# Optimization experiments

Hardware: AMD Instinct MI355X
Metric: run time of the kernel (lower is better)

## Reference

```python
import jax, jax.numpy as jnp
import numpy as np

DIM = 1024
NUM_HEADS = 16
HEAD_DIM = DIM // NUM_HEADS
SCALE = HEAD_DIM ** -0.5


def setup_inputs() -> dict:
    key = jax.random.key(0)
    ks = jax.random.split(key, 7)
    s = DIM ** -0.5
    return {
        "x": jax.random.normal(ks[0], (4, 2048, DIM), dtype=jnp.float32),
        "wq": jax.random.normal(ks[1], (DIM, DIM), dtype=jnp.float32) * s,
        "wk": jax.random.normal(ks[2], (DIM, DIM), dtype=jnp.float32) * s,
        "wv": jax.random.normal(ks[3], (DIM, DIM), dtype=jnp.float32) * s,
        "wo": jax.random.normal(ks[4], (DIM, DIM), dtype=jnp.float32) * s,
        "bo": jax.random.normal(ks[5], (DIM,), dtype=jnp.float32) * 0.02,
    }


def reference(x, wq, wk, wv, wo, bo):
    B, N, C = x.shape
    H, D = NUM_HEADS, HEAD_DIM
    # projections (qkv_bias=False); weights stored as [out, in] like nn.Linear
    q = jnp.einsum("bnc,oc->bno", x, wq).reshape(B, N, H, D).transpose(0, 2, 1, 3)
    k = jnp.einsum("bnc,oc->bno", x, wk).reshape(B, N, H, D).transpose(0, 2, 1, 3)
    v = jnp.einsum("bnc,oc->bno", x, wv).reshape(B, N, H, D).transpose(0, 2, 1, 3)
    # full NxN scores, scaled after the matmul as in the original
    scores = jnp.einsum("bhqd,bhkd->bhqk", q, k) * SCALE
    probs = jax.nn.softmax(scores, axis=-1)  # attn_drop is identity (p=0, eval)
    out = jnp.einsum("bhqk,bhkd->bhqd", probs, v)
    out = out.transpose(0, 2, 1, 3).reshape(B, N, C)
    # output projection with bias; proj_drop identity
    return jnp.einsum("bnc,oc->bno", out, wo) + bo
```

## Files before the change

kernel.cpp:

```cpp
#include <hip/hip_runtime.h>

typedef unsigned short u16;
typedef __attribute__((ext_vector_type(8))) short short8;
typedef __attribute__((ext_vector_type(4))) float f32x4;
typedef __attribute__((ext_vector_type(2))) unsigned u32x2;
typedef __attribute__((ext_vector_type(4))) unsigned u32x4;

#define LOG2E 1.44269504088896340736f

__device__ __forceinline__ u16 f2bf(float f) {
    unsigned u = __float_as_uint(f);
    u += 0x7fffu + ((u >> 16) & 1u);
    return (u16)(u >> 16);
}

__device__ __forceinline__ void async_cp16(const void* g, void* l) {
    __builtin_amdgcn_global_load_lds(
        (const __attribute__((address_space(1))) unsigned*)g,
        (__attribute__((address_space(3))) unsigned*)l, 16, 0, 0);
}

__device__ __forceinline__ unsigned pack_trunc(float a, float b) {
    return __builtin_amdgcn_perm(__float_as_uint(b), __float_as_uint(a), 0x07060302u);
}

__global__ void cast_all(const float4* __restrict__ x,
                         const float4* __restrict__ wq, const float4* __restrict__ wk,
                         const float4* __restrict__ wv, const float4* __restrict__ wo,
                         uint2* __restrict__ xb, uint2* __restrict__ wqkv,
                         uint2* __restrict__ wob) {
    long long g = (long long)blockIdx.x * blockDim.x + threadIdx.x;
    const long long XG = (8192LL * 1024) / 4;
    const long long WN = (1024LL * 1024) / 4;
    float4 v;
    uint2* dst;
    if (g < XG) {
        v = x[g];
        dst = xb + g;
    } else {
        long long t = g - XG;
        int s = (int)(t / WN);
        long long r = t - (long long)s * WN;
        const float4* src = (s == 0) ? wq : (s == 1) ? wk : (s == 2) ? wv : wo;
        v = src[r];
        dst = (s < 3) ? (wqkv + (long long)s * WN + r) : (wob + r);
    }
    uint2 p;
    p.x = (unsigned)f2bf(v.x) | ((unsigned)f2bf(v.y) << 16);
    p.y = (unsigned)f2bf(v.z) | ((unsigned)f2bf(v.w) << 16);
    *dst = p;
}

template <int MODE>
__global__ __launch_bounds__(256, 2) void gemm_nt(
    const u16* __restrict__ A, const u16* __restrict__ Bw,
    u16* __restrict__ Qo, u16* __restrict__ Ko, u16* __restrict__ Vto,
    float* __restrict__ Fo, const float* __restrict__ bias, int K) {
    __shared__ u16 As[128 * 64];
    __shared__ u16 Bs[128 * 64];

    const int tid = threadIdx.x;
    const int lane = tid & 63, wave = tid >> 6;
    const int wm = wave >> 1, wn = wave & 1;
    const int quad = lane >> 4, l16 = lane & 15;
    const long long m0 = (long long)blockIdx.x * 128;
    const long long n0 = (long long)blockIdx.y * 128;

    f32x4 acc[4][4];
#pragma unroll
    for (int i = 0; i < 4; i++)
#pragma unroll
        for (int j = 0; j < 4; j++) acc[i][j] = (f32x4){0.f, 0.f, 0.f, 0.f};

    for (int kt = 0; kt < K; kt += 64) {
#pragma unroll
        for (int i = 0; i < 4; i++) {
            int ff = i * 256 + tid;
            int row = ff >> 3, c = ff & 7;
            int gc = c ^ (row & 7);
            async_cp16(A + (m0 + row) * K + kt + gc * 8, &As[ff * 8]);
            async_cp16(Bw + (n0 + row) * K + kt + gc * 8, &Bs[ff * 8]);
        }
        __syncthreads();
#pragma unroll
        for (int ks = 0; ks < 2; ks++) {
            short8 af[4], bfr[4];
#pragma unroll
            for (int t = 0; t < 4; t++) {
                int rowA = wm * 64 + t * 16 + l16;
                int ca = (ks * 4 + quad) ^ (rowA & 7);
                af[t] = *(const short8*)(&As[rowA * 64 + ca * 8]);
                int rowB = wn * 64 + t * 16 + l16;
                int cb = (ks * 4 + quad) ^ (rowB & 7);
                bfr[t] = *(const short8*)(&Bs[rowB * 64 + cb * 8]);
            }
#pragma unroll
            for (int i = 0; i < 4; i++)
#pragma unroll
                for (int j = 0; j < 4; j++)
                    acc[i][j] = __builtin_amdgcn_mfma_f32_16x16x32_bf16(
                        af[i], bfr[j], acc[i][j], 0, 0, 0);
        }
        __syncthreads();
    }

#pragma unroll
    for (int i = 0; i < 4; i++) {
        int mg = (int)m0 + wm * 64 + i * 16 + quad * 4;
#pragma unroll
        for (int j = 0; j < 4; j++) {
            int ng = (int)n0 + wn * 64 + j * 16 + l16;
            f32x4 v = acc[i][j];
            if (MODE == 0) {
                int which = ng >> 10;
                int wi = ng & 1023;
                int h = wi >> 6, d = wi & 63;
                int b = mg >> 11;
                int seq = mg & 2047;
                long long bh = (long long)(b * 16 + h);
                if (which == 0) {
                    const float QS = 0.125f * LOG2E;
                    u16* dst = Qo + (bh * 2048 + seq) * 64 + d;
#pragma unroll
                    for (int r = 0; r < 4; r++) dst[r * 64] = f2bf(v[r] * QS);
                } else if (which == 1) {
                    u16* dst = Ko + (bh * 2048 + seq) * 64 + d;
#pragma unroll
                    for (int r = 0; r < 4; r++) dst[r * 64] = f2bf(v[r]);
                } else {
                    u16* dst = Vto + (bh * 64 + d) * 2048 + seq;
                    uint2 p;
                    p.x = (unsigned)f2bf(v[0]) | ((unsigned)f2bf(v[1]) << 16);
                    p.y = (unsigned)f2bf(v[2]) | ((unsigned)f2bf(v[3]) << 16);
                    *(uint2*)dst = p;
                }
            } else {
                float* dst = Fo + (long long)mg * 1024 + ng;
                float bb = bias[ng];
#pragma unroll
                for (int r = 0; r < 4; r++) dst[r * 1024] = v[r] + bb;
            }
        }
    }
}

__global__ __launch_bounds__(512, 4) void attn(
    const u16* __restrict__ Q, const u16* __restrict__ Kb,
    const u16* __restrict__ Vt, u16* __restrict__ O) {
    __shared__ u16 Ks[2][128 * 64];
    __shared__ u16 Vs[2][128 * 64];

    const int tid = threadIdx.x;
    const int lane = tid & 63, wave = tid >> 6;
    const int quad = lane >> 4, l16 = lane & 15;
    const int qt = blockIdx.y, bh = blockIdx.x;

    const u16* Qh = Q + (long long)bh * 2048 * 64;
    const u16* Kh = Kb + (long long)bh * 2048 * 64;
    const u16* Vh = Vt + (long long)bh * 64 * 2048;
    const int q0 = qt * 256 + wave * 32;

    const int srow = tid >> 3, sc = tid & 7;
    const int sgc = sc ^ (srow & 7);
    const u16* Kg = Kh + srow * 64 + sgc * 8;
    const u16* Vg = Vh + (long long)srow * 2048 + sgc * 8;

    short8 qf[2][2];
#pragma unroll
    for (int tm = 0; tm < 2; tm++)
#pragma unroll
        for (int ks = 0; ks < 2; ks++)
            qf[tm][ks] = *(const short8*)(Qh + (q0 + tm * 16 + l16) * 64 + ks * 32 + quad * 8);

    int kvo[2][4];
#pragma unroll
    for (int ks = 0; ks < 2; ks++)
#pragma unroll
        for (int tn = 0; tn < 4; tn++) {
            int row = tn * 16 + l16;
            kvo[ks][tn] = row * 64 + (((ks * 4 + quad) ^ (row & 7)) * 8);
        }

    f32x4 o_acc[2][4], lacc[2];
#pragma unroll
    for (int tm = 0; tm < 2; tm++) {
        lacc[tm] = (f32x4){0.f, 0.f, 0.f, 0.f};
#pragma unroll
        for (int tn = 0; tn < 4; tn++) o_acc[tm][tn] = (f32x4){0.f, 0.f, 0.f, 0.f};
    }
    const float NEGC = -12.0f * LOG2E;
    const short BF1 = (short)0x3F80;
    const short8 ones = {BF1, BF1, BF1, BF1, BF1, BF1, BF1, BF1};

    async_cp16(Kg, &Ks[0][tid * 8]);
    async_cp16(Kg + 4096, &Ks[0][4096 + tid * 8]);
    async_cp16(Vg, &Vs[0][tid * 8]);
    async_cp16(Vg + 64, &Vs[0][4096 + tid * 8]);

#define ATTN_HALF(KC, VC)                                                               \
    do {                                                                                \
        const u16* Kc = (KC);                                                           \
        const u16* Vc = (VC);                                                           \
        f32x4 s[2][4];                                                                  \
        _Pragma("unroll") for (int tm = 0; tm < 2; tm++)                                \
            _Pragma("unroll") for (int tn = 0; tn < 4; tn++)                            \
                s[tm][tn] = (f32x4){NEGC, NEGC, NEGC, NEGC};                            \
        _Pragma("unroll") for (int ks = 0; ks < 2; ks++) {                              \
            short8 kf[4];                                                               \
            _Pragma("unroll") for (int tn = 0; tn < 4; tn++)                            \
                kf[tn] = *(const short8*)(&Kc[kvo[ks][tn]]);                            \
            _Pragma("unroll") for (int tm = 0; tm < 2; tm++)                            \
                _Pragma("unroll") for (int tn = 0; tn < 4; tn++)                        \
                    s[tm][tn] = __builtin_amdgcn_mfma_f32_16x16x32_bf16(                \
                        kf[tn], qf[tm][ks], s[tm][tn], 0, 0, 0);                        \
        }                                                                               \
        short8 pa[2][2];                                                                \
        _Pragma("unroll") for (int tm = 0; tm < 2; tm++) {                              \
            unsigned W[4][2];                                                           \
            _Pragma("unroll") for (int tn = 0; tn < 4; tn++) {                          \
                f32x4 sv = s[tm][tn];                                                   \
                float e0 = __builtin_amdgcn_exp2f(sv[0]);                               \
                float e1 = __builtin_amdgcn_exp2f(sv[1]);                               \
                float e2 = __builtin_amdgcn_exp2f(sv[2]);                               \
                float e3 = __builtin_amdgcn_exp2f(sv[3]);                               \
                W[tn][0] = pack_trunc(e0, e1);                                          \
                W[tn][1] = pack_trunc(e2, e3);                                          \
            }                                                                           \
            _Pragma("unroll") for (int t2 = 0; t2 < 2; t2++)                            \
                _Pragma("unroll") for (int w = 0; w < 2; w++) {                         \
                    u32x2 r = __builtin_amdgcn_permlane32_swap(                         \
                        W[2 * t2][w], W[2 * t2 + 1][w], false, false);                  \
                    W[2 * t2][w] = r[0];                                                \
                    W[2 * t2 + 1][w] = r[1];                                            \
                }                                                                       \
            _Pragma("unroll") for (int t2 = 0; t2 < 2; t2++)                            \
                _Pragma("unroll") for (int w = 0; w < 2; w++) {                         \
                    u32x2 r = __builtin_amdgcn_permlane16_swap(                         \
                        W[2 * t2][w], W[2 * t2 + 1][w], false, false);                  \
                    W[2 * t2][w] = r[0];                                                \
                    W[2 * t2 + 1][w] = r[1];                                            \
                }                                                                       \
            _Pragma("unroll") for (int ks = 0; ks < 2; ks++) {                          \
                u32x4 pd;                                                               \
                pd[0] = W[2 * ks][0];                                                   \
                pd[1] = W[2 * ks][1];                                                   \
                pd[2] = W[2 * ks + 1][0];                                               \
                pd[3] = W[2 * ks + 1][1];                                               \
                pa[tm][ks] = *(short8*)&pd;                                             \
            }                                                                           \
        }                                                                               \
        _Pragma("unroll") for (int ks = 0; ks < 2; ks++) {                              \
            short8 vf[4];                                                               \
            _Pragma("unroll") for (int tn = 0; tn < 4; tn++)                            \
                vf[tn] = *(const short8*)(&Vc[kvo[ks][tn]]);                            \
            lacc[0] = __builtin_amdgcn_mfma_f32_16x16x32_bf16(pa[0][ks], ones, lacc[0], 0, 0, 0); \
            lacc[1] = __builtin_amdgcn_mfma_f32_16x16x32_bf16(pa[1][ks], ones, lacc[1], 0, 0, 0); \
            _Pragma("unroll") for (int tn = 0; tn < 4; tn++) {                          \
                o_acc[0][tn] = __builtin_amdgcn_mfma_f32_16x16x32_bf16(                 \
                    pa[0][ks], vf[tn], o_acc[0][tn], 0, 0, 0);                          \
                o_acc[1][tn] = __builtin_amdgcn_mfma_f32_16x16x32_bf16(                 \
                    pa[1][ks], vf[tn], o_acc[1][tn], 0, 0, 0);                          \
            }                                                                           \
        }                                                                               \
    } while (0)

#define ATTN_STEP(KT2, BUF)                                                             \
    do {                                                                                \
        __syncthreads();                                                                \
        if ((KT2) < 15) {                                                               \
            async_cp16(Kg + ((KT2) + 1) * 8192, &Ks[(BUF) ^ 1][tid * 8]);               \
            async_cp16(Kg + ((KT2) + 1) * 8192 + 4096, &Ks[(BUF) ^ 1][4096 + tid * 8]); \
            async_cp16(Vg + ((KT2) + 1) * 128, &Vs[(BUF) ^ 1][tid * 8]);                \
            async_cp16(Vg + ((KT2) + 1) * 128 + 64, &Vs[(BUF) ^ 1][4096 + tid * 8]);    \
        }                                                                               \
        ATTN_HALF(&Ks[BUF][0], &Vs[BUF][0]);                                            \
        ATTN_HALF(&Ks[BUF][4096], &Vs[BUF][4096]);                                      \
    } while (0)

#pragma unroll 1
    for (int kt2 = 0; kt2 < 16; kt2 += 2) {
        ATTN_STEP(kt2, 0);
        ATTN_STEP(kt2 + 1, 1);
    }
#undef ATTN_STEP
#undef ATTN_HALF

    f32x4 linv[2];
#pragma unroll
    for (int tm = 0; tm < 2; tm++)
#pragma unroll
        for (int r = 0; r < 4; r++) linv[tm][r] = 1.0f / lacc[tm][r];

    const int b = bh >> 4, h = bh & 15;
#pragma unroll
    for (int tm = 0; tm < 2; tm++)
#pragma unroll
        for (int tn = 0; tn < 4; tn++) {
            int seq = q0 + tm * 16 + quad * 4;
            int c = h * 64 + tn * 16 + l16;
            u16* dst = O + ((long long)(b * 2048 + seq)) * 1024 + c;
#pragma unroll
            for (int r = 0; r < 4; r++)
                dst[r * 1024] = f2bf(o_acc[tm][tn][r] * linv[tm][r]);
        }
}

extern "C" void kernel_launch(void* const* d_in, const int* in_sizes, int n_in,
                              void* d_out, int out_size, void* d_ws, size_t ws_size,
                              hipStream_t stream) {
    const float* x = (const float*)d_in[0];
    const float* wq = (const float*)d_in[1];
    const float* wk = (const float*)d_in[2];
    const float* wv = (const float*)d_in[3];
    const float* wo = (const float*)d_in[4];
    const float* bo = (const float*)d_in[5];
    float* out = (float*)d_out;

    char* ws = (char*)d_ws;
    u16* xb   = (u16*)(ws);
    u16* wqkv = (u16*)(ws + (16LL << 20));
    u16* wob  = (u16*)(ws + (22LL << 20));
    u16* Qb   = (u16*)(ws + (24LL << 20));
    u16* Kbuf = (u16*)(ws + (40LL << 20));
    u16* Vt   = (u16*)(ws + (56LL << 20));
    u16* Ob   = (u16*)(ws + (72LL << 20));

    cast_all<<<12288, 256, 0, stream>>>((const float4*)x, (const float4*)wq,
                                        (const float4*)wk, (const float4*)wv,
                                        (const float4*)wo, (uint2*)xb,
                                        (uint2*)wqkv, (uint2*)wob);

    dim3 g1(64, 24);
    gemm_nt<0><<<g1, 256, 0, stream>>>(xb, wqkv, Qb, Kbuf, Vt, nullptr, nullptr, 1024);

    dim3 g2(64, 8);
    attn<<<g2, 512, 0, stream>>>(Qb, Kbuf, Vt, Ob);

    dim3 g3(64, 8);
    gemm_nt<1><<<g3, 256, 0, stream>>>(Ob, wob, nullptr, nullptr, nullptr, out, bo, 1024);
}
```

Measured before the change: 244.0 us.

## Double-buffer LDS tiles in the projection GEMM to overlap loads with MFMA

The bf16 NT GEMM used for the QKV and output projections now keeps two LDS buffers for the A and B tiles. It prefetches the next K-slice with async global-to-LDS copies while the MFMAs run on the current slice, and drops the trailing barrier in each K iteration. The aim is to hide global memory latency behind compute. LDS use per block doubles to 64 KB, which could limit occupancy alongside the launch bound of 2 blocks.

```diff
diff --git a/kernel.cpp b/kernel.cpp
--- a/kernel.cpp
+++ b/kernel.cpp
@@ -56,8 +56,8 @@
     const u16* __restrict__ A, const u16* __restrict__ Bw,
     u16* __restrict__ Qo, u16* __restrict__ Ko, u16* __restrict__ Vto,
     float* __restrict__ Fo, const float* __restrict__ bias, int K) {
-    __shared__ u16 As[128 * 64];
-    __shared__ u16 Bs[128 * 64];
+    __shared__ u16 As[2][128 * 64];
+    __shared__ u16 Bs[2][128 * 64];
 
     const int tid = threadIdx.x;
     const int lane = tid & 63, wave = tid >> 6;
@@ -72,16 +72,23 @@
 #pragma unroll
         for (int j = 0; j < 4; j++) acc[i][j] = (f32x4){0.f, 0.f, 0.f, 0.f};
 
+#define GEMM_STAGE(BUF, KT)                                                     \
+    do {                                                                        \
+        _Pragma("unroll") for (int i = 0; i < 4; i++) {                         \
+            int ff = i * 256 + tid;                                             \
+            int row = ff >> 3, c = ff & 7;                                      \
+            int gc = c ^ (row & 7);                                             \
+            async_cp16(A + (m0 + row) * K + (KT) + gc * 8, &As[BUF][ff * 8]);   \
+            async_cp16(Bw + (n0 + row) * K + (KT) + gc * 8, &Bs[BUF][ff * 8]);  \
+        }                                                                       \
+    } while (0)
+
+    GEMM_STAGE(0, 0);
+
     for (int kt = 0; kt < K; kt += 64) {
-#pragma unroll
-        for (int i = 0; i < 4; i++) {
-            int ff = i * 256 + tid;
-            int row = ff >> 3, c = ff & 7;
-            int gc = c ^ (row & 7);
-            async_cp16(A + (m0 + row) * K + kt + gc * 8, &As[ff * 8]);
-            async_cp16(Bw + (n0 + row) * K + kt + gc * 8, &Bs[ff * 8]);
-        }
+        const int buf = (kt >> 6) & 1;
         __syncthreads();
+        if (kt + 64 < K) GEMM_STAGE(buf ^ 1, kt + 64);
 #pragma unroll
         for (int ks = 0; ks < 2; ks++) {
             short8 af[4], bfr[4];
@@ -89,10 +96,10 @@
             for (int t = 0; t < 4; t++) {
                 int rowA = wm * 64 + t * 16 + l16;
                 int ca = (ks * 4 + quad) ^ (rowA & 7);
-                af[t] = *(const short8*)(&As[rowA * 64 + ca * 8]);
+                af[t] = *(const short8*)(&As[buf][rowA * 64 + ca * 8]);
                 int rowB = wn * 64 + t * 16 + l16;
                 int cb = (ks * 4 + quad) ^ (rowB & 7);
-                bfr[t] = *(const short8*)(&Bs[rowB * 64 + cb * 8]);
+                bfr[t] = *(const short8*)(&Bs[buf][rowB * 64 + cb * 8]);
             }
 #pragma unroll
             for (int i = 0; i < 4; i++)
@@ -101,8 +108,8 @@
                     acc[i][j] = __builtin_amdgcn_mfma_f32_16x16x32_bf16(
                         af[i], bfr[j], acc[i][j], 0, 0, 0);
         }
-        __syncthreads();
-    }
+    }
+#undef GEMM_STAGE
 
 #pragma unroll
     for (int i = 0; i < 4; i++) {
```

Result: slower. 251.4 us (+3.0%).
